# Optimization experiments

Hardware: AMD Instinct MI355X
Metric: run time of the kernel (lower is better)

Reference implementation:

```python
import jax, jax.numpy as jnp
import numpy as np

B, S, H, P = 512, 256, 768, 32

def setup_inputs() -> dict:
    key = jax.random.key(0)
    k1, k2, k3, k4, k5, k6, k7, k8, k9 = jax.random.split(key, 9)
    physical_features_vec = jax.random.normal(k1, (B, S, H), dtype=jnp.float32)
    process_vec = jax.random.normal(k2, (B, S, H), dtype=jnp.float32)
    mirco_vec = jax.random.normal(k3, (B, S, H), dtype=jnp.float32)
    pos = jax.random.randint(k4, (B, P), 0, S, dtype=jnp.int64)
    # -1 padding (ragged lengths); keep column 0 always valid
    drop = jax.random.uniform(k5, (B, P)) < 0.3
    drop = drop.at[:, 0].set(False)
    alloy_pos = jnp.where(drop, jnp.int64(-1), pos)
    # Linear params (torch convention: W [out, in]), kaiming-uniform-ish init
    lim1 = 1.0 / np.sqrt(3 * H)
    W1 = jax.random.uniform(k6, (H, 3 * H), minval=-lim1, maxval=lim1, dtype=jnp.float32)
    b1 = jax.random.uniform(k7, (H,), minval=-lim1, maxval=lim1, dtype=jnp.float32)
    lim2 = 1.0 / np.sqrt(2 * H)
    W2 = jax.random.uniform(k8, (H, 2 * H), minval=-lim2, maxval=lim2, dtype=jnp.float32)
    b2 = jax.random.uniform(k9, (H,), minval=-lim2, maxval=lim2, dtype=jnp.float32)
    return {"physical_features_vec": physical_features_vec, "process_vec": process_vec,
            "mirco_vec": mirco_vec, "alloy_pos": alloy_pos,
            "W1": W1, "b1": b1, "W2": W2, "b2": b2}

def vec_pool(word_vec, pos):
    # masked gather + mean over valid positions (pos == -1 is padding)
    mask = pos != -1                                   # [B, P]
    safe = jnp.where(mask, pos, 0)                     # [B, P]
    gathered = jnp.take_along_axis(word_vec, safe[:, :, None], axis=1)  # [B, P, H]
    m = mask.astype(word_vec.dtype)[:, :, None]
    s = jnp.sum(gathered * m, axis=1)                  # [B, H]
    cnt = jnp.sum(m, axis=1)                           # [B, 1]
    return s / cnt

def l2norm(x, eps=1e-12):
    n = jnp.sqrt(jnp.sum(x * x, axis=1, keepdims=True))
    return x / jnp.maximum(n, eps)

def reference(physical_features_vec, process_vec, mirco_vec, alloy_pos, W1, b1, W2, b2):
    phys_sent = physical_features_vec[:, 0, :]
    pooled_proc = vec_pool(process_vec, alloy_pos)
    proc_sent = process_vec[:, 0, :]
    combined = jnp.concatenate([pooled_proc, proc_sent, phys_sent], axis=1)  # [B, 3H]
    combined = combined @ W1.T + b1
    normalized_combined = l2norm(combined)
    pooled_micro = vec_pool(mirco_vec, alloy_pos)
    micro_sent = mirco_vec[:, 0, :]
    micro = jnp.concatenate([pooled_micro, micro_sent], axis=1)  # [B, 2H]
    micro = micro @ W2.T + b2
    normalized_micro = l2norm(micro)
    return (normalized_combined, normalized_micro)
```

## Files before the change

### kernel.cpp

```cpp
#include <hip/hip_runtime.h>
#include <hip/hip_bf16.h>

#define B_  512
#define S_  256
#define H_  768
#define P_  32
#define K1_ 2304
#define K2_ 1536
#define N_  768
#define M_  512
#define NK1 72
#define NK2 48
#define CVT_BLOCKS 512

typedef __attribute__((ext_vector_type(8))) short bf16x8v;
typedef __attribute__((ext_vector_type(8))) unsigned short u16x8;
typedef __attribute__((ext_vector_type(4))) float f32x4v;

__device__ inline unsigned short bfb(float x) {
  __hip_bfloat16 h = __float2bfloat16(x);
  return *reinterpret_cast<unsigned short*>(&h);
}


__device__ inline void store4_frag(__hip_bfloat16* __restrict__ buf, int NK,
                                   int m, int k, float4 v) {
  int m16 = m >> 4, mr = m & 15, k32 = k >> 5, kg = (k >> 3) & 3, e = k & 7;
  size_t off = ((size_t)(m16 * NK + k32) * 64 + kg * 16 + mr) * 8 + e;
  ushort4 u;
  u.x = bfb(v.x); u.y = bfb(v.y); u.z = bfb(v.z); u.w = bfb(v.w);
  *reinterpret_cast<ushort4*>(buf + off) = u;
}

__global__ __launch_bounds__(192) void pool_cvt_kernel(
    const float* __restrict__ phys, const float* __restrict__ proc,
    const float* __restrict__ micro, const int* __restrict__ pos,
    const float* __restrict__ W1, const float* __restrict__ W2,
    __hip_bfloat16* __restrict__ A1f, __hip_bfloat16* __restrict__ A2f,
    __hip_bfloat16* __restrict__ W1f, __hip_bfloat16* __restrict__ W2f) {
  const int t = threadIdx.x;
  const int NPOOL = 2 * B_;
  if (blockIdx.x < NPOOL) {
    const int bid = blockIdx.x;
    const int x = bid & 7;
    const int r2 = bid >> 3;
    const int e = r2 & 3;
    const int sghi = r2 >> 2;
    const int sg = sghi * 8 + x;
    const int rsub = sg & 3;
    const int selm = sg >> 2;
    const int sel = selm >> 5;
    const int m16 = selm & 31;
    const int b = m16 * 16 + rsub * 4 + e;

    __shared__ int sp[P_];
    __shared__ int scnt;
    if (t < 64) {
      int p = (t < P_) ? pos[b * P_ + t] : -1;
      bool valid = (p != -1);
      unsigned long long m = __ballot(valid);
      int pre = __popcll(m & ((1ull << t) - 1ull));
      if (valid) sp[pre] = p;
      if (t == 0) scnt = (int)__popcll(m);
    }
    __syncthreads();
    const int c = scnt;
    const float inv = 1.0f / (float)c;

    const int H4 = H_ / 4;
    const float* base = (sel == 0) ? proc : micro;
    const float4* srcb = (const float4*)(base + (size_t)b * S_ * H_);

    float4 sent = srcb[t];
    float4 sph = make_float4(0.f, 0.f, 0.f, 0.f);
    if (sel == 0) sph = ((const float4*)(phys + (size_t)b * S_ * H_))[t];

    float4 s0 = make_float4(0.f, 0.f, 0.f, 0.f);
    float4 s1 = make_float4(0.f, 0.f, 0.f, 0.f);
    int i = 0;
    for (; i + 8 <= c; i += 8) {
      float4 v0 = srcb[(size_t)sp[i+0] * H4 + t];
      float4 v1 = srcb[(size_t)sp[i+1] * H4 + t];
      float4 v2 = srcb[(size_t)sp[i+2] * H4 + t];
      float4 v3 = srcb[(size_t)sp[i+3] * H4 + t];
      float4 v4 = srcb[(size_t)sp[i+4] * H4 + t];
      float4 v5 = srcb[(size_t)sp[i+5] * H4 + t];
      float4 v6 = srcb[(size_t)sp[i+6] * H4 + t];
      float4 v7 = srcb[(size_t)sp[i+7] * H4 + t];
      s0.x += v0.x + v1.x + v2.x + v3.x;  s1.x += v4.x + v5.x + v6.x + v7.x;
      s0.y += v0.y + v1.y + v2.y + v3.y;  s1.y += v4.y + v5.y + v6.y + v7.y;
      s0.z += v0.z + v1.z + v2.z + v3.z;  s1.z += v4.z + v5.z + v6.z + v7.z;
      s0.w += v0.w + v1.w + v2.w + v3.w;  s1.w += v4.w + v5.w + v6.w + v7.w;
    }
    for (; i + 2 <= c; i += 2) {
      float4 v0 = srcb[(size_t)sp[i+0] * H4 + t];
      float4 v1 = srcb[(size_t)sp[i+1] * H4 + t];
      s0.x += v0.x + v1.x; s0.y += v0.y + v1.y;
      s0.z += v0.z + v1.z; s0.w += v0.w + v1.w;
    }
    if (i < c) {
      float4 v = srcb[(size_t)sp[i] * H4 + t];
      s0.x += v.x; s0.y += v.y; s0.z += v.z; s0.w += v.w;
    }
    float4 pooled = make_float4((s0.x + s1.x) * inv, (s0.y + s1.y) * inv,
                                (s0.z + s1.z) * inv, (s0.w + s1.w) * inv);

    const int k = t * 4;
    if (sel == 0) {
      store4_frag(A1f, NK1, b, k,          pooled);
      store4_frag(A1f, NK1, b, k + H_,     sent);
      store4_frag(A1f, NK1, b, k + 2*H_,   sph);
    } else {
      store4_frag(A2f, NK2, b, k,          pooled);
      store4_frag(A2f, NK2, b, k + H_,     sent);
    }
  } else {
    const int NG1 = 48 * NK1 * 64;
    const int NG2 = 48 * NK2 * 64;
    int tid = (blockIdx.x - NPOOL) * 192 + t;
    const int stride = CVT_BLOCKS * 192;
    for (int g = tid; g < NG1 + NG2; g += stride) {
      const float* W; __hip_bfloat16* Wf; int NK, K, gg;
      if (g < NG1) { W = W1; Wf = W1f; NK = NK1; K = K1_; gg = g; }
      else         { W = W2; Wf = W2f; NK = NK2; K = K2_; gg = g - NG1; }
      int lane = gg & 63;
      int rest = gg >> 6;
      int k32 = rest % NK;
      int n16 = rest / NK;
      int n = n16 * 16 + (lane & 15);
      int k = k32 * 32 + (lane >> 4) * 8;
      const float4* sW = (const float4*)(W + (size_t)n * K + k);
      float4 v0 = sW[0], v1 = sW[1];
      u16x8 o;
      o[0] = bfb(v0.x); o[1] = bfb(v0.y); o[2] = bfb(v0.z); o[3] = bfb(v0.w);
      o[4] = bfb(v1.x); o[5] = bfb(v1.y); o[6] = bfb(v1.z); o[7] = bfb(v1.w);
      *reinterpret_cast<u16x8*>(Wf + (size_t)gg * 8) = o;
    }
  }
}

#define MFMA4(A0V, A1V, W0V, W1V)                                             \
  acc00 = __builtin_amdgcn_mfma_f32_16x16x32_bf16(A0V, W0V, acc00, 0, 0, 0);  \
  acc01 = __builtin_amdgcn_mfma_f32_16x16x32_bf16(A0V, W1V, acc01, 0, 0, 0);  \
  acc10 = __builtin_amdgcn_mfma_f32_16x16x32_bf16(A1V, W0V, acc10, 0, 0, 0);  \
  acc11 = __builtin_amdgcn_mfma_f32_16x16x32_bf16(A1V, W1V, acc11, 0, 0, 0);

template <int NK>
__device__ inline void gemm_body(const bf16x8v* __restrict__ Af,
                                 const bf16x8v* __restrict__ Wf,
                                 const float* __restrict__ bias,
                                 float* __restrict__ C, int mt, int nt) {
  const int lane = threadIdx.x & 63;

  const bf16x8v* A0 = Af + (size_t)(2 * mt) * NK * 64 + lane;
  const bf16x8v* A1 = A0 + (size_t)NK * 64;
  const bf16x8v* B0 = Wf + (size_t)(2 * nt) * NK * 64 + lane;
  const bf16x8v* B1 = B0 + (size_t)NK * 64;

  f32x4v acc00 = {0.f, 0.f, 0.f, 0.f};
  f32x4v acc01 = {0.f, 0.f, 0.f, 0.f};
  f32x4v acc10 = {0.f, 0.f, 0.f, 0.f};
  f32x4v acc11 = {0.f, 0.f, 0.f, 0.f};

  bf16x8v a0s0 = A0[0],  a1s0 = A1[0],  w0s0 = B0[0],  w1s0 = B1[0];
  bf16x8v a0s1 = A0[64], a1s1 = A1[64], w0s1 = B0[64], w1s1 = B1[64];

  for (int k = 0; k < NK - 2; k += 2) {
    bf16x8v pa0 = A0[(size_t)(k + 2) * 64];
    bf16x8v pa1 = A1[(size_t)(k + 2) * 64];
    bf16x8v pw0 = B0[(size_t)(k + 2) * 64];
    bf16x8v pw1 = B1[(size_t)(k + 2) * 64];
    bf16x8v qa0 = A0[(size_t)(k + 3) * 64];
    bf16x8v qa1 = A1[(size_t)(k + 3) * 64];
    bf16x8v qw0 = B0[(size_t)(k + 3) * 64];
    bf16x8v qw1 = B1[(size_t)(k + 3) * 64];
    MFMA4(a0s0, a1s0, w0s0, w1s0)
    MFMA4(a0s1, a1s1, w0s1, w1s1)
    a0s0 = pa0; a1s0 = pa1; w0s0 = pw0; w1s0 = pw1;
    a0s1 = qa0; a1s1 = qa1; w0s1 = qw0; w1s1 = qw1;
  }
  MFMA4(a0s0, a1s0, w0s0, w1s0)
  MFMA4(a0s1, a1s1, w0s1, w1s1)

  const int m0 = mt * 32, n0 = nt * 32;
  const int col = lane & 15;
  const int rg = (lane >> 4) * 4;
  const float bv0 = bias[n0 + col];
  const float bv1 = bias[n0 + 16 + col];
#pragma unroll
  for (int j = 0; j < 4; ++j) {
    const int r = rg + j;
    C[(size_t)(m0 + r) * N_ + n0 + col]           = acc00[j] + bv0;
    C[(size_t)(m0 + r) * N_ + n0 + 16 + col]      = acc01[j] + bv1;
    C[(size_t)(m0 + 16 + r) * N_ + n0 + col]      = acc10[j] + bv0;
    C[(size_t)(m0 + 16 + r) * N_ + n0 + 16 + col] = acc11[j] + bv1;
  }
}

__global__ __launch_bounds__(256) void gemm_mfma_kernel(
    const __hip_bfloat16* __restrict__ A1f, const __hip_bfloat16* __restrict__ A2f,
    const __hip_bfloat16* __restrict__ W1f, const __hip_bfloat16* __restrict__ W2f,
    const float* __restrict__ b1, const float* __restrict__ b2,
    float* __restrict__ out) {
  const int bid = blockIdx.x;
  const int x = bid & 7;
  const int local = bid >> 3;
  const int ntb_g = x * 3 + local % 3;
  const int mtb = local / 3;
  const int wid = threadIdx.x >> 6;
  const int wr = wid >> 1, wc = wid & 1;
  const int mt = mtb * 2 + wr;
  if (ntb_g < 12) {
    const int nt = ntb_g * 2 + wc;
    gemm_body<NK1>((const bf16x8v*)A1f, (const bf16x8v*)W1f, b1, out, mt, nt);
  } else {
    const int nt = (ntb_g - 12) * 2 + wc;
    gemm_body<NK2>((const bf16x8v*)A2f, (const bf16x8v*)W2f, b2,
                   out + (size_t)M_ * N_, mt, nt);
  }
}

__global__ __launch_bounds__(256) void norm_rows_kernel(float* __restrict__ out) {
  const int row = blockIdx.x;
  float* p = out + (size_t)row * N_;
  const int t = threadIdx.x;
  float x0 = p[t];
  float x1 = p[t + 256];
  float x2 = p[t + 512];
  float s = x0*x0 + x1*x1 + x2*x2;
#pragma unroll
  for (int off = 32; off > 0; off >>= 1) s += __shfl_down(s, off);
  __shared__ float ws[4];
  const int lane = t & 63, wid = t >> 6;
  if (lane == 0) ws[wid] = s;
  __syncthreads();
  float tot = ws[0] + ws[1] + ws[2] + ws[3];
  float inv = 1.0f / fmaxf(sqrtf(tot), 1e-12f);
  p[t]       = x0 * inv;
  p[t + 256] = x1 * inv;
  p[t + 512] = x2 * inv;
}

extern "C" void kernel_launch(void* const* d_in, const int* in_sizes, int n_in,
                              void* d_out, int out_size, void* d_ws, size_t ws_size,
                              hipStream_t stream) {
  const float* phys  = (const float*)d_in[0];
  const float* proc  = (const float*)d_in[1];
  const float* micro = (const float*)d_in[2];
  const int*   pos   = (const int*)d_in[3];
  const float* W1    = (const float*)d_in[4];
  const float* b1    = (const float*)d_in[5];
  const float* W2    = (const float*)d_in[6];
  const float* b2    = (const float*)d_in[7];
  float* out = (float*)d_out;

  __hip_bfloat16* A1f = (__hip_bfloat16*)d_ws;
  __hip_bfloat16* A2f = A1f + (size_t)32 * NK1 * 512;
  __hip_bfloat16* W1f = A2f + (size_t)32 * NK2 * 512;
  __hip_bfloat16* W2f = W1f + (size_t)48 * NK1 * 512;

  pool_cvt_kernel<<<2 * B_ + CVT_BLOCKS, 192, 0, stream>>>(
      phys, proc, micro, pos, W1, W2, A1f, A2f, W1f, W2f);
  gemm_mfma_kernel<<<192, 256, 0, stream>>>(
      A1f, A2f, W1f, W2f, b1, b2, out);
  norm_rows_kernel<<<2 * B_, 256, 0, stream>>>(out);
}
```

Before: 45.41 us.

## Fuse row L2-norm into GEMM via last-block-done atomic counter

Removes the separate norm kernel launch. Each GEMM block bumps a per-row-group atomic counter after storing its tile, and the last of the 12 blocks covering that row band normalizes the 64 rows in place. Counters are zeroed by the preceding pool/convert kernel. The pool block index mapping is also simplified to b=bid>>1, sel=bid&1. In exchange, the normalization is serialized onto a few blocks at the tail, and the change relies on relaxed atomics plus vmcnt waits for memory visibility.

```diff
diff --git a/kernel.cpp b/kernel.cpp
--- a/kernel.cpp
+++ b/kernel.cpp
@@ -22,7 +22,6 @@
   return *reinterpret_cast<unsigned short*>(&h);
 }
 
-
 __device__ inline void store4_frag(__hip_bfloat16* __restrict__ buf, int NK,
                                    int m, int k, float4 v) {
   int m16 = m >> 4, mr = m & 15, k32 = k >> 5, kg = (k >> 3) & 3, e = k & 7;
@@ -32,26 +31,36 @@
   *reinterpret_cast<ushort4*>(buf + off) = u;
 }
 
+__device__ inline void cvt_one(const float* __restrict__ W,
+                               __hip_bfloat16* __restrict__ Wf,
+                               int NK, int K, int gg) {
+  int lane = gg & 63;
+  int rest = gg >> 6;
+  int k32 = rest % NK;
+  int n16 = rest / NK;
+  int n = n16 * 16 + (lane & 15);
+  int k = k32 * 32 + (lane >> 4) * 8;
+  const float4* sW = (const float4*)(W + (size_t)n * K + k);
+  float4 v0 = sW[0], v1 = sW[1];
+  u16x8 o;
+  o[0] = bfb(v0.x); o[1] = bfb(v0.y); o[2] = bfb(v0.z); o[3] = bfb(v0.w);
+  o[4] = bfb(v1.x); o[5] = bfb(v1.y); o[6] = bfb(v1.z); o[7] = bfb(v1.w);
+  *reinterpret_cast<u16x8*>(Wf + (size_t)gg * 8) = o;
+}
+
 __global__ __launch_bounds__(192) void pool_cvt_kernel(
     const float* __restrict__ phys, const float* __restrict__ proc,
     const float* __restrict__ micro, const int* __restrict__ pos,
     const float* __restrict__ W1, const float* __restrict__ W2,
     __hip_bfloat16* __restrict__ A1f, __hip_bfloat16* __restrict__ A2f,
-    __hip_bfloat16* __restrict__ W1f, __hip_bfloat16* __restrict__ W2f) {
+    __hip_bfloat16* __restrict__ W1f, __hip_bfloat16* __restrict__ W2f,
+    int* __restrict__ cnt) {
   const int t = threadIdx.x;
   const int NPOOL = 2 * B_;
   if (blockIdx.x < NPOOL) {
     const int bid = blockIdx.x;
-    const int x = bid & 7;
-    const int r2 = bid >> 3;
-    const int e = r2 & 3;
-    const int sghi = r2 >> 2;
-    const int sg = sghi * 8 + x;
-    const int rsub = sg & 3;
-    const int selm = sg >> 2;
-    const int sel = selm >> 5;
-    const int m16 = selm & 31;
-    const int b = m16 * 16 + rsub * 4 + e;
+    const int b   = bid >> 1;
+    const int sel = bid & 1;
 
     __shared__ int sp[P_];
     __shared__ int scnt;
@@ -115,26 +124,14 @@
       store4_frag(A2f, NK2, b, k + H_,     sent);
     }
   } else {
+    if (blockIdx.x == NPOOL && t < 16) cnt[t] = 0;
     const int NG1 = 48 * NK1 * 64;
     const int NG2 = 48 * NK2 * 64;
     int tid = (blockIdx.x - NPOOL) * 192 + t;
     const int stride = CVT_BLOCKS * 192;
     for (int g = tid; g < NG1 + NG2; g += stride) {
-      const float* W; __hip_bfloat16* Wf; int NK, K, gg;
-      if (g < NG1) { W = W1; Wf = W1f; NK = NK1; K = K1_; gg = g; }
-      else         { W = W2; Wf = W2f; NK = NK2; K = K2_; gg = g - NG1; }
-      int lane = gg & 63;
-      int rest = gg >> 6;
-      int k32 = rest % NK;
-      int n16 = rest / NK;
-      int n = n16 * 16 + (lane & 15);
-      int k = k32 * 32 + (lane >> 4) * 8;
-      const float4* sW = (const float4*)(W + (size_t)n * K + k);
-      float4 v0 = sW[0], v1 = sW[1];
-      u16x8 o;
-      o[0] = bfb(v0.x); o[1] = bfb(v0.y); o[2] = bfb(v0.z); o[3] = bfb(v0.w);
-      o[4] = bfb(v1.x); o[5] = bfb(v1.y); o[6] = bfb(v1.z); o[7] = bfb(v1.w);
-      *reinterpret_cast<u16x8*>(Wf + (size_t)gg * 8) = o;
+      if (g < NG1) cvt_one(W1, W1f, NK1, K1_, g);
+      else         cvt_one(W2, W2f, NK2, K2_, g - NG1);
     }
   }
 }
@@ -190,55 +187,70 @@
 #pragma unroll
   for (int j = 0; j < 4; ++j) {
     const int r = rg + j;
-    C[(size_t)(m0 + r) * N_ + n0 + col]           = acc00[j] + bv0;
-    C[(size_t)(m0 + r) * N_ + n0 + 16 + col]      = acc01[j] + bv1;
-    C[(size_t)(m0 + 16 + r) * N_ + n0 + col]      = acc10[j] + bv0;
-    C[(size_t)(m0 + 16 + r) * N_ + n0 + 16 + col] = acc11[j] + bv1;
-  }
-}
-
-__global__ __launch_bounds__(256) void gemm_mfma_kernel(
+    __hip_atomic_store(&C[(size_t)(m0 + r) * N_ + n0 + col], acc00[j] + bv0,
+                       __ATOMIC_RELAXED, __HIP_MEMORY_SCOPE_AGENT);
+    __hip_atomic_store(&C[(size_t)(m0 + r) * N_ + n0 + 16 + col], acc01[j] + bv1,
+                       __ATOMIC_RELAXED, __HIP_MEMORY_SCOPE_AGENT);
+    __hip_atomic_store(&C[(size_t)(m0 + 16 + r) * N_ + n0 + col], acc10[j] + bv0,
+                       __ATOMIC_RELAXED, __HIP_MEMORY_SCOPE_AGENT);
+    __hip_atomic_store(&C[(size_t)(m0 + 16 + r) * N_ + n0 + 16 + col], acc11[j] + bv1,
+                       __ATOMIC_RELAXED, __HIP_MEMORY_SCOPE_AGENT);
+  }
+}
+
+__global__ __launch_bounds__(256) void gemm_norm_kernel(
     const __hip_bfloat16* __restrict__ A1f, const __hip_bfloat16* __restrict__ A2f,
     const __hip_bfloat16* __restrict__ W1f, const __hip_bfloat16* __restrict__ W2f,
     const float* __restrict__ b1, const float* __restrict__ b2,
-    float* __restrict__ out) {
+    float* __restrict__ out, int* __restrict__ cnt) {
   const int bid = blockIdx.x;
   const int x = bid & 7;
   const int local = bid >> 3;
   const int ntb_g = x * 3 + local % 3;
   const int mtb = local / 3;
   const int wid = threadIdx.x >> 6;
+  const int lane = threadIdx.x & 63;
   const int wr = wid >> 1, wc = wid & 1;
   const int mt = mtb * 2 + wr;
-  if (ntb_g < 12) {
+  const bool g2 = (ntb_g >= 12);
+  float* Cg = g2 ? out + (size_t)M_ * N_ : out;
+  if (!g2) {
     const int nt = ntb_g * 2 + wc;
-    gemm_body<NK1>((const bf16x8v*)A1f, (const bf16x8v*)W1f, b1, out, mt, nt);
+    gemm_body<NK1>((const bf16x8v*)A1f, (const bf16x8v*)W1f, b1, Cg, mt, nt);
   } else {
     const int nt = (ntb_g - 12) * 2 + wc;
-    gemm_body<NK2>((const bf16x8v*)A2f, (const bf16x8v*)W2f, b2,
-                   out + (size_t)M_ * N_, mt, nt);
-  }
-}
-
-__global__ __launch_bounds__(256) void norm_rows_kernel(float* __restrict__ out) {
-  const int row = blockIdx.x;
-  float* p = out + (size_t)row * N_;
-  const int t = threadIdx.x;
-  float x0 = p[t];
-  float x1 = p[t + 256];
-  float x2 = p[t + 512];
-  float s = x0*x0 + x1*x1 + x2*x2;
-#pragma unroll
-  for (int off = 32; off > 0; off >>= 1) s += __shfl_down(s, off);
-  __shared__ float ws[4];
-  const int lane = t & 63, wid = t >> 6;
-  if (lane == 0) ws[wid] = s;
+    gemm_body<NK2>((const bf16x8v*)A2f, (const bf16x8v*)W2f, b2, Cg, mt, nt);
+  }
+
+  __shared__ int sdone;
+  asm volatile("s_waitcnt vmcnt(0)" ::: "memory");
   __syncthreads();
-  float tot = ws[0] + ws[1] + ws[2] + ws[3];
-  float inv = 1.0f / fmaxf(sqrtf(tot), 1e-12f);
-  p[t]       = x0 * inv;
-  p[t + 256] = x1 * inv;
-  p[t + 512] = x2 * inv;
+  const int rgid = (g2 ? 8 : 0) + mtb;
+  if (threadIdx.x == 0) {
+    int prev = __hip_atomic_fetch_add(&cnt[rgid], 1, __ATOMIC_RELAXED,
+                                      __HIP_MEMORY_SCOPE_AGENT);
+    sdone = (prev == 11);
+  }
+  __syncthreads();
+  if (!sdone) return;
+
+  const int r0 = mtb * 64 + wid * 16;
+  for (int rr = 0; rr < 16; ++rr) {
+    float* p = Cg + (size_t)(r0 + rr) * N_;
+    float v[12];
+    float ss = 0.f;
+#pragma unroll
+    for (int e = 0; e < 12; ++e) {
+      v[e] = __hip_atomic_load(&p[e * 64 + lane], __ATOMIC_RELAXED,
+                               __HIP_MEMORY_SCOPE_AGENT);
+      ss += v[e] * v[e];
+    }
+#pragma unroll
+    for (int off = 32; off > 0; off >>= 1) ss += __shfl_xor(ss, off);
+    const float inv = 1.0f / fmaxf(sqrtf(ss), 1e-12f);
+#pragma unroll
+    for (int e = 0; e < 12; ++e) p[e * 64 + lane] = v[e] * inv;
+  }
 }
 
 extern "C" void kernel_launch(void* const* d_in, const int* in_sizes, int n_in,
@@ -258,10 +270,10 @@
   __hip_bfloat16* A2f = A1f + (size_t)32 * NK1 * 512;
   __hip_bfloat16* W1f = A2f + (size_t)32 * NK2 * 512;
   __hip_bfloat16* W2f = W1f + (size_t)48 * NK1 * 512;
+  int* cnt = (int*)(W2f + (size_t)48 * NK2 * 512);
 
   pool_cvt_kernel<<<2 * B_ + CVT_BLOCKS, 192, 0, stream>>>(
-      phys, proc, micro, pos, W1, W2, A1f, A2f, W1f, W2f);
-  gemm_mfma_kernel<<<192, 256, 0, stream>>>(
-      A1f, A2f, W1f, W2f, b1, b2, out);
-  norm_rows_kernel<<<2 * B_, 256, 0, stream>>>(out);
-}
+      phys, proc, micro, pos, W1, W2, A1f, A2f, W1f, W2f, cnt);
+  gemm_norm_kernel<<<192, 256, 0, stream>>>(
+      A1f, A2f, W1f, W2f, b1, b2, out, cnt);
+}
```

Result: slower. 51.14 us (+12.6%).
